# Optimization experiments

Hardware: AMD Instinct MI355X
Metric: run time of the kernel (lower is better)

## Reference

```python
import jax, jax.numpy as jnp
import numpy as np

D, H, WIN, TEMP = 512, 8, 2, 1.0
DH = D // H
SCALE = DH ** -0.5
SHIFT = WIN // 2


def _ln(x, g, b):
    m = jnp.mean(x, -1, keepdims=True)
    v = jnp.mean(jnp.square(x - m), -1, keepdims=True)
    return (x - m) * jax.lax.rsqrt(v + 1e-5) * g + b


def _win_attn(q, k, v):
    a = jax.nn.softmax(jnp.einsum('nhqd,nhkd->nhqk', q * SCALE, k) / TEMP, axis=-1)
    return jnp.einsum('nhqk,nhkd->nhqd', a, v)


def _self_block(x, p):
    qkv_w, qkv_b, proj_w, proj_b, n1g, n1b, n2g, n2b = p
    b, t, d = x.shape
    sc = x
    xw = _ln(x, n1g, n1b).reshape(b * t // WIN, WIN, d)  # window partition
    qkv = (xw @ qkv_w + qkv_b).reshape(-1, WIN, 3, H, DH).transpose(2, 0, 3, 1, 4)
    o = _win_attn(qkv[0], qkv[1], qkv[2])
    o = o.transpose(0, 2, 1, 3).reshape(-1, WIN, d) @ proj_w + proj_b
    return _ln(o.reshape(b, t, d) + sc, n2g, n2b)  # window reverse + residual


def _self_tf(x, p):
    x = _self_block(x, p)
    x = jnp.roll(x, -SHIFT, axis=1)   # sequence_shift
    x = _self_block(x, p)
    return jnp.roll(x, SHIFT, axis=1)  # sequence_inverse_shift


def _cross_block(x, y, p):
    q_w, q_b, kv_w, kv_b, proj_w, proj_b, n1g, n1b, n2g, n2b = p
    b, t, d = x.shape
    sc = x
    xw = _ln(x, n1g, n1b).reshape(-1, WIN, d)
    yw = _ln(y, n1g, n1b).reshape(-1, WIN, d)  # shared pre_norm, as in source
    q = (xw @ q_w + q_b).reshape(-1, WIN, H, DH).transpose(0, 2, 1, 3)
    kv = (yw @ kv_w + kv_b).reshape(-1, WIN, 2, H, DH).transpose(2, 0, 3, 1, 4)
    o = _win_attn(q, kv[0], kv[1])
    o = o.transpose(0, 2, 1, 3).reshape(-1, WIN, d) @ proj_w + proj_b
    return _ln(o.reshape(b, t, d) + sc, n2g, n2b)


def _cross_tf(x, y, p):
    x = _cross_block(x, y, p)
    x = jnp.roll(x, -SHIFT, axis=1)
    x = _cross_block(x, jnp.roll(y, -SHIFT, axis=1), p)
    return jnp.roll(x, SHIFT, axis=1)


def setup_inputs() -> dict:
    key = jax.random.key(0)
    ks = iter(jax.random.split(key, 40))
    B, T = 16, 4096
    d = {
        'x': jax.random.normal(next(ks), (B, T, D), jnp.float32),
        'y': jax.random.normal(next(ks), (B, T, D), jnp.float32),
    }

    def w(shape):
        return jax.random.normal(next(ks), shape, jnp.float32) * 0.02

    for m in ('wa', 'wv'):  # within-modal audio / video
        d[m + '_qkv_w'] = w((D, 3 * D)); d[m + '_qkv_b'] = jnp.zeros((3 * D,), jnp.float32)
        d[m + '_proj_w'] = w((D, D));    d[m + '_proj_b'] = jnp.zeros((D,), jnp.float32)
        d[m + '_n1_g'] = jnp.ones((D,), jnp.float32); d[m + '_n1_b'] = jnp.zeros((D,), jnp.float32)
        d[m + '_n2_g'] = jnp.ones((D,), jnp.float32); d[m + '_n2_b'] = jnp.zeros((D,), jnp.float32)
    # shared cross-modal transformer
    d['cm_q_w'] = w((D, D));      d['cm_q_b'] = jnp.zeros((D,), jnp.float32)
    d['cm_kv_w'] = w((D, 2 * D)); d['cm_kv_b'] = jnp.zeros((2 * D,), jnp.float32)
    d['cm_proj_w'] = w((D, D));   d['cm_proj_b'] = jnp.zeros((D,), jnp.float32)
    d['cm_n1_g'] = jnp.ones((D,), jnp.float32); d['cm_n1_b'] = jnp.zeros((D,), jnp.float32)
    d['cm_n2_g'] = jnp.ones((D,), jnp.float32); d['cm_n2_b'] = jnp.zeros((D,), jnp.float32)
    return d


def reference(x, y,
              wa_qkv_w, wa_qkv_b, wa_proj_w, wa_proj_b, wa_n1_g, wa_n1_b, wa_n2_g, wa_n2_b,
              wv_qkv_w, wv_qkv_b, wv_proj_w, wv_proj_b, wv_n1_g, wv_n1_b, wv_n2_g, wv_n2_b,
              cm_q_w, cm_q_b, cm_kv_w, cm_kv_b, cm_proj_w, cm_proj_b, cm_n1_g, cm_n1_b, cm_n2_g, cm_n2_b):
    pa = (wa_qkv_w, wa_qkv_b, wa_proj_w, wa_proj_b, wa_n1_g, wa_n1_b, wa_n2_g, wa_n2_b)
    pv = (wv_qkv_w, wv_qkv_b, wv_proj_w, wv_proj_b, wv_n1_g, wv_n1_b, wv_n2_g, wv_n2_b)
    pc = (cm_q_w, cm_q_b, cm_kv_w, cm_kv_b, cm_proj_w, cm_proj_b, cm_n1_g, cm_n1_b, cm_n2_g, cm_n2_b)
    # args.s1_attn == 'all' path
    x = _self_tf(x, pa)
    y = _self_tf(y, pv)
    xc = _cross_tf(x, y, pc)
    yc = _cross_tf(y, x, pc)
    return jnp.stack([x + xc, y + yc])  # (2, B, T, D)
```

## Files before the change

kernel.cpp:

```cpp
#include <hip/hip_runtime.h>

typedef unsigned short u16;
typedef unsigned int u32;
typedef __attribute__((ext_vector_type(8))) short short8;
typedef __attribute__((ext_vector_type(4))) short short4v;
typedef __attribute__((ext_vector_type(4))) float f32x4;

#define D_MODEL 512
#define NH 8
#define TSEQ 4096
#define NB 16
#define NROWS (NB*TSEQ)
#define QK_SCALE 0.125f
#define KDIM 512
#define NKI (KDIM/32)

__device__ __forceinline__ float b2f(u16 u){
    union { float f; unsigned int i; } v; v.i = ((unsigned int)u) << 16; return v.f;
}
__device__ __forceinline__ u16 f2b(float f){
    union { float f; unsigned int i; } v; v.f = f;
    unsigned int r = v.i + 0x7FFFu + ((v.i >> 16) & 1u);
    return (u16)(r >> 16);
}

__device__ __forceinline__ void async_copy16(u16* lds, const u16* g){
    __builtin_amdgcn_global_load_lds(
        (const __attribute__((address_space(1))) u32*)g,
        (__attribute__((address_space(3))) u32*)lds, 16, 0, 0);
}

__global__ void wconv_kernel(const float* __restrict__ W, u16* __restrict__ Wt, int K, int N){
    int idx = blockIdx.x * 256 + threadIdx.x;
    if (idx >= K * N) return;
    int n = idx / K;
    int k = idx - n * K;
    Wt[idx] = f2b(W[(size_t)k * N + n]);
}

__global__ __launch_bounds__(256) void ln_kernel(
    const float* __restrict__ X, const float* __restrict__ g,
    const float* __restrict__ b, u16* __restrict__ out)
{
    int row  = blockIdx.x * 4 + (threadIdx.x >> 6);
    int lane = threadIdx.x & 63;
    size_t base = (size_t)row * D_MODEL + lane * 8;
    float4 x0 = *(const float4*)(X + base);
    float4 x1 = *(const float4*)(X + base + 4);
    float t[8] = {x0.x,x0.y,x0.z,x0.w,x1.x,x1.y,x1.z,x1.w};
    float s = 0.f, ss = 0.f;
    #pragma unroll
    for (int j = 0; j < 8; j++){ s += t[j]; ss += t[j]*t[j]; }
    #pragma unroll
    for (int m = 1; m < 64; m <<= 1){ s += __shfl_xor(s, m); ss += __shfl_xor(ss, m); }
    float mean = s * (1.f/D_MODEL);
    float var  = ss * (1.f/D_MODEL) - mean*mean;
    float rst  = rsqrtf(var + 1e-5f);
    float4 g0 = *(const float4*)(g + lane*8);
    float4 g1 = *(const float4*)(g + lane*8 + 4);
    float4 c0 = *(const float4*)(b + lane*8);
    float4 c1 = *(const float4*)(b + lane*8 + 4);
    float gv[8] = {g0.x,g0.y,g0.z,g0.w,g1.x,g1.y,g1.z,g1.w};
    float bv[8] = {c0.x,c0.y,c0.z,c0.w,c1.x,c1.y,c1.z,c1.w};
    short8 o;
    #pragma unroll
    for (int j = 0; j < 8; j++) o[j] = (short)f2b((t[j]-mean)*rst*gv[j] + bv[j]);
    *(short8*)(out + base) = o;
}

__global__ __launch_bounds__(256) void resln_kernel(
    const u16* __restrict__ P, const float* __restrict__ Xin,
    const float* __restrict__ Add,
    const float* __restrict__ g, const float* __restrict__ b,
    float* __restrict__ out,
    u16* __restrict__ lnout, const float* __restrict__ g2, const float* __restrict__ b2)
{
    int row  = blockIdx.x * 4 + (threadIdx.x >> 6);
    int lane = threadIdx.x & 63;
    size_t base = (size_t)row * D_MODEL + lane * 8;
    short8 pv = *(const short8*)(P + base);
    float4 x0 = *(const float4*)(Xin + base);
    float4 x1 = *(const float4*)(Xin + base + 4);
    float xr[8] = {x0.x,x0.y,x0.z,x0.w,x1.x,x1.y,x1.z,x1.w};
    float t[8];
    #pragma unroll
    for (int j = 0; j < 8; j++) t[j] = b2f((u16)pv[j]) + xr[j];
    float s = 0.f, ss = 0.f;
    #pragma unroll
    for (int j = 0; j < 8; j++){ s += t[j]; ss += t[j]*t[j]; }
    #pragma unroll
    for (int m = 1; m < 64; m <<= 1){ s += __shfl_xor(s, m); ss += __shfl_xor(ss, m); }
    float mean = s * (1.f/D_MODEL);
    float var  = ss * (1.f/D_MODEL) - mean*mean;
    float rst  = rsqrtf(var + 1e-5f);
    float4 g0 = *(const float4*)(g + lane*8);
    float4 g1 = *(const float4*)(g + lane*8 + 4);
    float4 c0 = *(const float4*)(b + lane*8);
    float4 c1 = *(const float4*)(b + lane*8 + 4);
    float gv[8] = {g0.x,g0.y,g0.z,g0.w,g1.x,g1.y,g1.z,g1.w};
    float bv[8] = {c0.x,c0.y,c0.z,c0.w,c1.x,c1.y,c1.z,c1.w};
    float lnb[8], o[8];
    #pragma unroll
    for (int j = 0; j < 8; j++){ lnb[j] = (t[j]-mean)*rst; o[j] = lnb[j]*gv[j] + bv[j]; }

    if (lnout){
        float s2 = 0.f, ss2 = 0.f;
        #pragma unroll
        for (int j = 0; j < 8; j++){ s2 += o[j]; ss2 += o[j]*o[j]; }
        #pragma unroll
        for (int m = 1; m < 64; m <<= 1){ s2 += __shfl_xor(s2, m); ss2 += __shfl_xor(ss2, m); }
        float mean2 = s2 * (1.f/D_MODEL);
        float var2  = ss2 * (1.f/D_MODEL) - mean2*mean2;
        float rst2  = rsqrtf(var2 + 1e-5f);
        float4 g20 = *(const float4*)(g2 + lane*8);
        float4 g21 = *(const float4*)(g2 + lane*8 + 4);
        float4 b20 = *(const float4*)(b2 + lane*8);
        float4 b21 = *(const float4*)(b2 + lane*8 + 4);
        float g2v[8] = {g20.x,g20.y,g20.z,g20.w,g21.x,g21.y,g21.z,g21.w};
        float b2v[8] = {b20.x,b20.y,b20.z,b20.w,b21.x,b21.y,b21.z,b21.w};
        short8 lo;
        #pragma unroll
        for (int j = 0; j < 8; j++) lo[j] = (short)f2b((o[j]-mean2)*rst2*g2v[j] + b2v[j]);
        *(short8*)(lnout + base) = lo;
    }
    if (Add){
        float4 a0 = *(const float4*)(Add + base);
        float4 a1 = *(const float4*)(Add + base + 4);
        float av[8] = {a0.x,a0.y,a0.z,a0.w,a1.x,a1.y,a1.z,a1.w};
        #pragma unroll
        for (int j = 0; j < 8; j++) o[j] += av[j];
    }
    float4 r0 = {o[0],o[1],o[2],o[3]};
    float4 r1 = {o[4],o[5],o[6],o[7]};
    *(float4*)(out + base)     = r0;
    *(float4*)(out + base + 4) = r1;
}

__global__ __launch_bounds__(256) void qkvattn_kernel(
    const u16* __restrict__ A, const u16* __restrict__ Wt,
    const float* __restrict__ bias, u16* __restrict__ O, int shift)
{
    __shared__ __align__(16) u16 lds[2][20*512];
    int tid  = threadIdx.x;
    int lane = tid & 63;
    int wid  = tid >> 6;

    int bid  = blockIdx.x;
    int swz  = (bid & 7) * 512 + (bid >> 3);
    int head = swz >> 9;
    int rt   = swz & 511;
    int bt   = rt >> 5;
    int tb   = (rt & 31) * 128;

    f32x4 acc[2][12];
    f32x4 zero = {0.f,0.f,0.f,0.f};
    #pragma unroll
    for (int m = 0; m < 2; m++)
        #pragma unroll
        for (int n = 0; n < 12; n++) acc[m][n] = zero;

    int rr = lane >> 2, kc = (lane & 3) * 8;
    const u16* p[5];
    int cidb = wid * 5;
    #pragma unroll
    for (int q = 0; q < 5; q++){
        int cid = cidb + q;
        if (cid < 8){
            int i   = cid*16 + rr;
            int tok = (tb + shift + i) & (TSEQ-1);
            p[q] = A + ((size_t)bt * TSEQ + tok) * KDIM + kc;
        } else {
            int cb   = cid - 8;
            int wrow = (cb >> 2) * 512 + head*64 + (cb & 3)*16 + rr;
            p[q] = Wt + (size_t)wrow * KDIM + kc;
        }
    }

    int lrow = lane & 15;
    int lk   = (lane >> 4) * 8;
    int aoff = (wid*32 + lrow) * 32 + lk;
    int boff = 8*512 + lrow*32 + lk;

    #pragma unroll
    for (int q = 0; q < 5; q++){ async_copy16(&lds[0][(cidb+q)*512], p[q]); p[q] += 32; }
    asm volatile("s_waitcnt vmcnt(0)" ::: "memory");
    __syncthreads();

    #pragma unroll
    for (int t = 0; t < NKI; t++){
        const u16* cbuf = lds[t & 1];
        u16* nbuf = (u16*)lds[(t & 1) ^ 1];
        if (t < NKI-1){
            #pragma unroll
            for (int q = 0; q < 5; q++){ async_copy16(&nbuf[(cidb+q)*512], p[q]); p[q] += 32; }
        }
        short8 af[2], bf[12];
        #pragma unroll
        for (int m = 0; m < 2; m++) af[m] = *(const short8*)(cbuf + aoff + m*512);
        #pragma unroll
        for (int n = 0; n < 12; n++) bf[n] = *(const short8*)(cbuf + boff + n*512);
        #pragma unroll
        for (int m = 0; m < 2; m++)
            #pragma unroll
            for (int n = 0; n < 12; n++)
                acc[m][n] = __builtin_amdgcn_mfma_f32_16x16x32_bf16(af[m], bf[n], acc[m][n], 0, 0, 0);
        if (t < NKI-1){
            asm volatile("s_waitcnt vmcnt(0)" ::: "memory");
            __syncthreads();
        }
    }

    int g_ = lane >> 4, lc = lane & 15;
    float bq[4], bk[4], bv[4];
    #pragma unroll
    for (int n = 0; n < 4; n++){
        int d = head*64 + n*16 + lc;
        bq[n] = bias[d]; bk[n] = bias[512 + d]; bv[n] = bias[1024 + d];
    }
    #pragma unroll
    for (int m = 0; m < 2; m++){
        #pragma unroll
        for (int wnd = 0; wnd < 2; wnd++){
            int ja = 2*wnd, jb = ja + 1;
            float s00=0.f, s01=0.f, s10=0.f, s11=0.f;
            #pragma unroll
            for (int n = 0; n < 4; n++){
                float qa = acc[m][n][ja] + bq[n],  qb = acc[m][n][jb] + bq[n];
                float ka = acc[m][4+n][ja] + bk[n], kb = acc[m][4+n][jb] + bk[n];
                s00 += qa*ka; s01 += qa*kb; s10 += qb*ka; s11 += qb*kb;
            }
            #pragma unroll
            for (int msk = 1; msk < 16; msk <<= 1){
                s00 += __shfl_xor(s00, msk); s01 += __shfl_xor(s01, msk);
                s10 += __shfl_xor(s10, msk); s11 += __shfl_xor(s11, msk);
            }
            s00 *= QK_SCALE; s01 *= QK_SCALE; s10 *= QK_SCALE; s11 *= QK_SCALE;
            float m0 = fmaxf(s00, s01), m1 = fmaxf(s10, s11);
            float e00 = expf(s00-m0), e01 = expf(s01-m0);
            float e10 = expf(s10-m1), e11 = expf(s11-m1);
            float ia = 1.f/(e00+e01), ib = 1.f/(e10+e11);
            float a00 = e00*ia, a01 = e01*ia, a10 = e10*ib, a11 = e11*ib;
            int ra = wid*32 + m*16 + 4*g_ + ja;
            int ta = (tb + shift + ra) & (TSEQ-1);
            size_t growa = (size_t)bt * TSEQ + ta;
            size_t growb = (size_t)bt * TSEQ + ((ta + 1) & (TSEQ-1));
            #pragma unroll
            for (int n = 0; n < 4; n++){
                float va = acc[m][8+n][ja] + bv[n], vb = acc[m][8+n][jb] + bv[n];
                int col = head*64 + n*16 + lc;
                O[growa * D_MODEL + col] = f2b(a00*va + a01*vb);
                O[growb * D_MODEL + col] = f2b(a10*va + a11*vb);
            }
        }
    }
}

#define BM 128
#define BN 128

__global__ __launch_bounds__(256) void gemm_kernel(
    const u16* __restrict__ A, const u16* __restrict__ Wt,
    const float* __restrict__ bias, u16* __restrict__ C,
    int N, int nN)
{
    __shared__ __align__(16) u16 lds[2][16*512];
    int tid  = threadIdx.x;
    int lane = tid & 63;
    int wid  = tid >> 6;
    int wm = wid >> 1, wn = wid & 1;

    int cpx = (int)gridDim.x >> 3;
    int swz = ((int)blockIdx.x & 7) * cpx + ((int)blockIdx.x >> 3);
    int row0 = (swz / nN) * BM;
    int col0 = (swz % nN) * BN;

    f32x4 acc[4][4];
    f32x4 zero = {0.f,0.f,0.f,0.f};
    #pragma unroll
    for (int i = 0; i < 4; i++)
        #pragma unroll
        for (int j = 0; j < 4; j++) acc[i][j] = zero;

    int rr = lane >> 2, kc = (lane & 3) * 8;
    const u16* p[4];
    int cidb = wid * 4;
    #pragma unroll
    for (int q = 0; q < 4; q++){
        int cid = cidb + q;
        if (cid < 8) p[q] = A  + (size_t)(row0 + cid*16 + rr) * KDIM + kc;
        else         p[q] = Wt + (size_t)(col0 + (cid-8)*16 + rr) * KDIM + kc;
    }

    int lrow = lane & 15;
    int lk   = (lane >> 4) * 8;
    int aoff = (wm*64 + lrow) * 32 + lk;
    int boff = 8*512 + (wn*64 + lrow) * 32 + lk;

    #pragma unroll
    for (int q = 0; q < 4; q++){ async_copy16(&lds[0][(cidb+q)*512], p[q]); p[q] += 32; }
    asm volatile("s_waitcnt vmcnt(0)" ::: "memory");
    __syncthreads();

    #pragma unroll
    for (int t = 0; t < NKI; t++){
        const u16* cbuf = lds[t & 1];
        u16* nbuf = (u16*)lds[(t & 1) ^ 1];
        if (t < NKI-1){
            #pragma unroll
            for (int q = 0; q < 4; q++){ async_copy16(&nbuf[(cidb+q)*512], p[q]); p[q] += 32; }
        }
        short8 af[4], bf[4];
        #pragma unroll
        for (int m = 0; m < 4; m++) af[m] = *(const short8*)(cbuf + aoff + m*512);
        #pragma unroll
        for (int n = 0; n < 4; n++) bf[n] = *(const short8*)(cbuf + boff + n*512);
        #pragma unroll
        for (int m = 0; m < 4; m++)
            #pragma unroll
            for (int n = 0; n < 4; n++)
                acc[m][n] = __builtin_amdgcn_mfma_f32_16x16x32_bf16(af[m], bf[n], acc[m][n], 0, 0, 0);
        if (t < NKI-1){
            asm volatile("s_waitcnt vmcnt(0)" ::: "memory");
            __syncthreads();
        }
    }

    int lr4 = (lane >> 4) * 4;
    int lc  = lane & 15;
    #pragma unroll
    for (int n = 0; n < 4; n++) {
        int c = col0 + wn*64 + n*16 + lc;
        float bvv = bias[c];
        #pragma unroll
        for (int m = 0; m < 4; m++) {
            int r = row0 + wm*64 + m*16 + lr4;
            f32x4 v = acc[m][n];
            C[(size_t)(r+0) * N + c] = f2b(v[0] + bvv);
            C[(size_t)(r+1) * N + c] = f2b(v[1] + bvv);
            C[(size_t)(r+2) * N + c] = f2b(v[2] + bvv);
            C[(size_t)(r+3) * N + c] = f2b(v[3] + bvv);
        }
    }
}

__global__ __launch_bounds__(256) void attn_cross_kernel(
    const u16* __restrict__ Q, const u16* __restrict__ KV,
    u16* __restrict__ O, int shift)
{
    int tsk  = blockIdx.x * 4 + (threadIdx.x >> 6);
    int lane = threadIdx.x & 63;
    int w  = tsk >> 1;
    int hb = tsk & 1;
    int bt = w >> 11;
    int wt = w & 2047;
    int t0 = (2*wt + shift) & (TSEQ - 1);
    int t1 = (t0 + 1) & (TSEQ - 1);
    size_t g0 = (size_t)bt * TSEQ + t0;
    size_t g1 = (size_t)bt * TSEQ + t1;
    int col = hb*256 + lane*4;
    short4v q0 = *(const short4v*)(Q  + g0*512  + col);
    short4v q1 = *(const short4v*)(Q  + g1*512  + col);
    short4v k0 = *(const short4v*)(KV + g0*1024 + col);
    short4v k1 = *(const short4v*)(KV + g1*1024 + col);
    short4v v0 = *(const short4v*)(KV + g0*1024 + 512 + col);
    short4v v1 = *(const short4v*)(KV + g1*1024 + 512 + col);
    float s00=0.f, s01=0.f, s10=0.f, s11=0.f;
    float v0f[4], v1f[4];
    #pragma unroll
    for (int j = 0; j < 4; j++){
        float qa = b2f((u16)q0[j]), qb = b2f((u16)q1[j]);
        float ka = b2f((u16)k0[j]), kb = b2f((u16)k1[j]);
        v0f[j] = b2f((u16)v0[j]); v1f[j] = b2f((u16)v1[j]);
        s00 += qa*ka; s01 += qa*kb; s10 += qb*ka; s11 += qb*kb;
    }
    #pragma unroll
    for (int m = 1; m < 16; m <<= 1){
        s00 += __shfl_xor(s00, m); s01 += __shfl_xor(s01, m);
        s10 += __shfl_xor(s10, m); s11 += __shfl_xor(s11, m);
    }
    s00 *= QK_SCALE; s01 *= QK_SCALE; s10 *= QK_SCALE; s11 *= QK_SCALE;
    float m0 = fmaxf(s00, s01), m1 = fmaxf(s10, s11);
    float e00 = expf(s00 - m0), e01 = expf(s01 - m0);
    float e10 = expf(s10 - m1), e11 = expf(s11 - m1);
    float ia = 1.f/(e00 + e01), ib = 1.f/(e10 + e11);
    float a00 = e00*ia, a01 = e01*ia, a10 = e10*ib, a11 = e11*ib;
    short4v o0, o1;
    #pragma unroll
    for (int j = 0; j < 4; j++){
        o0[j] = (short)f2b(a00*v0f[j] + a01*v1f[j]);
        o1[j] = (short)f2b(a10*v0f[j] + a11*v1f[j]);
    }
    *(short4v*)(O + g0*512 + col) = o0;
    *(short4v*)(O + g1*512 + col) = o1;
}

extern "C" void kernel_launch(void* const* d_in, const int* in_sizes, int n_in,
                              void* d_out, int out_size, void* d_ws, size_t ws_size,
                              hipStream_t stream)
{
    const float* x = (const float*)d_in[0];
    const float* y = (const float*)d_in[1];
    const float* wa_qkv_w = (const float*)d_in[2];  const float* wa_qkv_b = (const float*)d_in[3];
    const float* wa_proj_w= (const float*)d_in[4];  const float* wa_proj_b= (const float*)d_in[5];
    const float* wa_n1g   = (const float*)d_in[6];  const float* wa_n1b   = (const float*)d_in[7];
    const float* wa_n2g   = (const float*)d_in[8];  const float* wa_n2b   = (const float*)d_in[9];
    const float* wv_qkv_w = (const float*)d_in[10]; const float* wv_qkv_b = (const float*)d_in[11];
    const float* wv_proj_w= (const float*)d_in[12]; const float* wv_proj_b= (const float*)d_in[13];
    const float* wv_n1g   = (const float*)d_in[14]; const float* wv_n1b   = (const float*)d_in[15];
    const float* wv_n2g   = (const float*)d_in[16]; const float* wv_n2b   = (const float*)d_in[17];
    const float* cm_q_w   = (const float*)d_in[18]; const float* cm_q_b   = (const float*)d_in[19];
    const float* cm_kv_w  = (const float*)d_in[20]; const float* cm_kv_b  = (const float*)d_in[21];
    const float* cm_proj_w= (const float*)d_in[22]; const float* cm_proj_b= (const float*)d_in[23];
    const float* cm_n1g   = (const float*)d_in[24]; const float* cm_n1b   = (const float*)d_in[25];
    const float* cm_n2g   = (const float*)d_in[26]; const float* cm_n2b   = (const float*)d_in[27];

    char* ws = (char*)d_ws;
    const size_t SZ_F32 = (size_t)NROWS * D_MODEL * 4;
    const size_t SZ_B16 = (size_t)NROWS * D_MODEL * 2;
    float* F1  = (float*)(ws);
    float* XF  = (float*)(ws + SZ_F32);
    float* YF  = (float*)(ws + 2*SZ_F32);
    u16*   XN  = (u16*)  (ws + 3*SZ_F32);
    u16*   CN  = (u16*)  (ws + 3*SZ_F32 + SZ_B16);
    u16*   XLN = (u16*)  (ws + 3*SZ_F32 + 2*SZ_B16);
    u16*   YLN = (u16*)  (ws + 3*SZ_F32 + 3*SZ_B16);
    u16*   O   = (u16*)  (ws + 3*SZ_F32 + 4*SZ_B16);
    u16*   KVb = (u16*)  (ws + 3*SZ_F32 + 5*SZ_B16);
    u16*   WB  = (u16*)  (ws + 3*SZ_F32 + 8*SZ_B16);

    u16* PB = KVb;

    u16* wa_qkv_t  = WB;
    u16* wa_proj_t = wa_qkv_t  + 1536*512;
    u16* wv_qkv_t  = wa_proj_t + 512*512;
    u16* wv_proj_t = wv_qkv_t  + 1536*512;
    u16* cm_q_t    = wv_proj_t + 512*512;
    u16* cm_kv_t   = cm_q_t    + 512*512;
    u16* cm_proj_t = cm_kv_t   + 1024*512;

    auto conv = [&](const float* W, u16* Wt, int K, int N){
        int total = K * N;
        wconv_kernel<<<(total + 255) / 256, 256, 0, stream>>>(W, Wt, K, N);
    };
    conv(wa_qkv_w,  wa_qkv_t,  512, 1536);
    conv(wa_proj_w, wa_proj_t, 512, 512);
    conv(wv_qkv_w,  wv_qkv_t,  512, 1536);
    conv(wv_proj_w, wv_proj_t, 512, 512);
    conv(cm_q_w,    cm_q_t,    512, 512);
    conv(cm_kv_w,   cm_kv_t,   512, 1024);
    conv(cm_proj_w, cm_proj_t, 512, 512);

    const int lnGrid   = NROWS / 4;
    const int attnGrid = NROWS / 2 * 2 / 4;
    const int qaGrid   = (NROWS / 128) * NH;

    auto gemm = [&](const u16* Ain, const u16* Wt, const float* bias, u16* Cout, int N){
        int nN = N / BN;
        gemm_kernel<<<(NROWS/BM) * nN, 256, 0, stream>>>(Ain, Wt, bias, Cout, N, nN);
    };

    auto self_chain = [&](const float* in, float* outF, u16* outLN,
                          const u16* qkvT, const float* qkv_b,
                          const u16* projT, const float* proj_b,
                          const float* n1g, const float* n1b,
                          const float* n2g, const float* n2b){
        ln_kernel<<<lnGrid, 256, 0, stream>>>(in, n1g, n1b, XN);
        qkvattn_kernel<<<qaGrid, 256, 0, stream>>>(XN, qkvT, qkv_b, O, 0);
        gemm(O, projT, proj_b, PB, 512);
        resln_kernel<<<lnGrid, 256, 0, stream>>>(PB, in, nullptr, n2g, n2b, F1, XN, n1g, n1b);
        qkvattn_kernel<<<qaGrid, 256, 0, stream>>>(XN, qkvT, qkv_b, O, 1);
        gemm(O, projT, proj_b, PB, 512);
        resln_kernel<<<lnGrid, 256, 0, stream>>>(PB, F1, nullptr, n2g, n2b, outF, outLN, cm_n1g, cm_n1b);
    };

    self_chain(x, XF, XLN, wa_qkv_t, wa_qkv_b, wa_proj_t, wa_proj_b, wa_n1g, wa_n1b, wa_n2g, wa_n2b);
    self_chain(y, YF, YLN, wv_qkv_t, wv_qkv_b, wv_proj_t, wv_proj_b, wv_n1g, wv_n1b, wv_n2g, wv_n2b);

    float* out0 = (float*)d_out;
    float* out1 = out0 + (size_t)NROWS * D_MODEL;

    auto cross_chain = [&](const u16* qLN, const u16* kvLN, const float* resF, float* outF){
        gemm(kvLN, cm_kv_t, cm_kv_b, KVb, 1024);
        gemm(qLN,  cm_q_t,  cm_q_b,  XN,  512);
        attn_cross_kernel<<<attnGrid, 256, 0, stream>>>(XN, KVb, O, 0);
        gemm(O, cm_proj_t, cm_proj_b, XN, 512);
        resln_kernel<<<lnGrid, 256, 0, stream>>>(XN, resF, nullptr, cm_n2g, cm_n2b, F1, CN, cm_n1g, cm_n1b);
        gemm(CN, cm_q_t, cm_q_b, XN, 512);
        attn_cross_kernel<<<attnGrid, 256, 0, stream>>>(XN, KVb, O, 1);
        gemm(O, cm_proj_t, cm_proj_b, XN, 512);
        resln_kernel<<<lnGrid, 256, 0, stream>>>(XN, F1, resF, cm_n2g, cm_n2b, outF, nullptr, nullptr, nullptr);
    };

    cross_chain(XLN, YLN, XF, out0);
    cross_chain(YLN, XLN, YF, out1);
}
```

Measured before the change: 2.372 ms.

## Replace 128x128 GEMM with 256x256 tiled, swizzled-LDS, 512-thread kernel

Replaces the projection GEMM with a kernel that computes 256x256 output tiles using 8 waves. Each wave holds an 8x4 grid of MFMA accumulators, and each pipeline stage loads K=64. LDS rows are XOR-swizzled to reduce bank conflicts, loads use a partial vmcnt wait, and MFMA issue is raised with setprio. The goal is more data reuse per loaded byte and fewer sync points per K step. In exchange it uses 128KB of LDS and more registers, which lowers occupancy, and it launches fewer blocks.

After: 2.495 ms. +5.2%, slower.

```diff
diff --git a/kernel.cpp b/kernel.cpp
--- a/kernel.cpp
+++ b/kernel.cpp
@@ -99,9 +99,9 @@
     float4 c1 = *(const float4*)(b + lane*8 + 4);
     float gv[8] = {g0.x,g0.y,g0.z,g0.w,g1.x,g1.y,g1.z,g1.w};
     float bv[8] = {c0.x,c0.y,c0.z,c0.w,c1.x,c1.y,c1.z,c1.w};
-    float lnb[8], o[8];
-    #pragma unroll
-    for (int j = 0; j < 8; j++){ lnb[j] = (t[j]-mean)*rst; o[j] = lnb[j]*gv[j] + bv[j]; }
+    float o[8];
+    #pragma unroll
+    for (int j = 0; j < 8; j++) o[j] = (t[j]-mean)*rst*gv[j] + bv[j];
 
     if (lnout){
         float s2 = 0.f, ss2 = 0.f;
@@ -255,85 +255,101 @@
     }
 }
 
-#define BM 128
-#define BN 128
-
-__global__ __launch_bounds__(256) void gemm_kernel(
+__global__ __launch_bounds__(512) void gemm256_kernel(
     const u16* __restrict__ A, const u16* __restrict__ Wt,
-    const float* __restrict__ bias, u16* __restrict__ C,
-    int N, int nN)
+    const float* __restrict__ bias, u16* __restrict__ C, int N, int nN)
 {
-    __shared__ __align__(16) u16 lds[2][16*512];
+    __shared__ __align__(16) u16 sh[65536];
     int tid  = threadIdx.x;
     int lane = tid & 63;
     int wid  = tid >> 6;
-    int wm = wid >> 1, wn = wid & 1;
+    int wm   = wid >> 2, wn = wid & 3;
 
     int cpx = (int)gridDim.x >> 3;
     int swz = ((int)blockIdx.x & 7) * cpx + ((int)blockIdx.x >> 3);
-    int row0 = (swz / nN) * BM;
-    int col0 = (swz % nN) * BN;
-
-    f32x4 acc[4][4];
+    int row0 = (swz / nN) * 256;
+    int col0 = (swz % nN) * 256;
+
+    f32x4 acc[8][4];
     f32x4 zero = {0.f,0.f,0.f,0.f};
     #pragma unroll
-    for (int i = 0; i < 4; i++)
-        #pragma unroll
-        for (int j = 0; j < 4; j++) acc[i][j] = zero;
-
-    int rr = lane >> 2, kc = (lane & 3) * 8;
-    const u16* p[4];
-    int cidb = wid * 4;
-    #pragma unroll
-    for (int q = 0; q < 4; q++){
-        int cid = cidb + q;
-        if (cid < 8) p[q] = A  + (size_t)(row0 + cid*16 + rr) * KDIM + kc;
-        else         p[q] = Wt + (size_t)(col0 + (cid-8)*16 + rr) * KDIM + kc;
-    }
-
-    int lrow = lane & 15;
-    int lk   = (lane >> 4) * 8;
-    int aoff = (wm*64 + lrow) * 32 + lk;
-    int boff = 8*512 + (wn*64 + lrow) * 32 + lk;
-
-    #pragma unroll
-    for (int q = 0; q < 4; q++){ async_copy16(&lds[0][(cidb+q)*512], p[q]); p[q] += 32; }
-    asm volatile("s_waitcnt vmcnt(0)" ::: "memory");
-    __syncthreads();
-
-    #pragma unroll
-    for (int t = 0; t < NKI; t++){
-        const u16* cbuf = lds[t & 1];
-        u16* nbuf = (u16*)lds[(t & 1) ^ 1];
-        if (t < NKI-1){
-            #pragma unroll
-            for (int q = 0; q < 4; q++){ async_copy16(&nbuf[(cidb+q)*512], p[q]); p[q] += 32; }
+    for (int m = 0; m < 8; m++)
+        #pragma unroll
+        for (int n = 0; n < 4; n++) acc[m][n] = zero;
+
+    int lrow = lane & 15, khi = lane >> 4;
+    int addrA[8], addrB[4];
+    #pragma unroll
+    for (int m = 0; m < 8; m++){
+        int r = wm*128 + m*16 + lrow;
+        addrA[m] = r*32 + ((khi ^ ((r>>1)&3)) << 3);
+    }
+    #pragma unroll
+    for (int n = 0; n < 4; n++){
+        int r = wn*64 + n*16 + lrow;
+        addrB[n] = r*32 + ((khi ^ ((r>>1)&3)) << 3);
+    }
+
+    const u16* Ab = A  + (size_t)row0 * KDIM;
+    const u16* Bb = Wt + (size_t)col0 * KDIM;
+    int sr0 = (wid << 4) + (lane >> 2);
+    int ss  = lane & 3;
+    int sx  = (ss ^ ((sr0 >> 1) & 3)) << 3;
+
+    #define STAGE_A(buf, t, kh) { \
+        u16* d_ = &sh[(buf)*16384 + (kh)*8192 + wid*512]; \
+        const u16* s_ = Ab + (size_t)sr0*KDIM + (t)*64 + (kh)*32 + sx; \
+        async_copy16(d_, s_); \
+        async_copy16(d_ + 4096, s_ + (size_t)128*KDIM); }
+    #define STAGE_B(buf, t, kh) { \
+        u16* d_ = &sh[32768 + (buf)*16384 + (kh)*8192 + wid*512]; \
+        const u16* s_ = Bb + (size_t)sr0*KDIM + (t)*64 + (kh)*32 + sx; \
+        async_copy16(d_, s_); \
+        async_copy16(d_ + 4096, s_ + (size_t)128*KDIM); }
+
+    #define COMPUTE(buf, kh) { \
+        const u16* ca_ = &sh[(buf)*16384 + (kh)*8192]; \
+        const u16* cb_ = ca_ + 32768; \
+        short8 af[8], bf[4]; \
+        _Pragma("unroll") \
+        for (int m = 0; m < 8; m++) af[m] = *(const short8*)(ca_ + addrA[m]); \
+        _Pragma("unroll") \
+        for (int n = 0; n < 4; n++) bf[n] = *(const short8*)(cb_ + addrB[n]); \
+        __builtin_amdgcn_s_setprio(1); \
+        _Pragma("unroll") \
+        for (int m = 0; m < 8; m++) \
+            _Pragma("unroll") \
+            for (int n = 0; n < 4; n++) \
+                acc[m][n] = __builtin_amdgcn_mfma_f32_16x16x32_bf16(af[m], bf[n], acc[m][n], 0, 0, 0); \
+        __builtin_amdgcn_s_setprio(0); }
+
+    STAGE_A(0, 0, 0); STAGE_B(0, 0, 0);
+    STAGE_A(0, 0, 1); STAGE_B(0, 0, 1);
+
+    #pragma unroll
+    for (int t = 0; t < 8; t++){
+        int buf = t & 1;
+        if (t < 7){
+            STAGE_A(buf^1, t+1, 0); STAGE_B(buf^1, t+1, 0);
+            STAGE_A(buf^1, t+1, 1); STAGE_B(buf^1, t+1, 1);
+            asm volatile("s_waitcnt vmcnt(8)" ::: "memory");
+        } else {
+            asm volatile("s_waitcnt vmcnt(0)" ::: "memory");
         }
-        short8 af[4], bf[4];
-        #pragma unroll
-        for (int m = 0; m < 4; m++) af[m] = *(const short8*)(cbuf + aoff + m*512);
-        #pragma unroll
-        for (int n = 0; n < 4; n++) bf[n] = *(const short8*)(cbuf + boff + n*512);
-        #pragma unroll
-        for (int m = 0; m < 4; m++)
-            #pragma unroll
-            for (int n = 0; n < 4; n++)
-                acc[m][n] = __builtin_amdgcn_mfma_f32_16x16x32_bf16(af[m], bf[n], acc[m][n], 0, 0, 0);
-        if (t < NKI-1){
-            asm volatile("s_waitcnt vmcnt(0)" ::: "memory");
-            __syncthreads();
-        }
-    }
-
-    int lr4 = (lane >> 4) * 4;
-    int lc  = lane & 15;
-    #pragma unroll
-    for (int n = 0; n < 4; n++) {
+        __builtin_amdgcn_s_barrier();
+        COMPUTE(buf, 0);
+        COMPUTE(buf, 1);
+        __builtin_amdgcn_s_barrier();
+    }
+
+    int g_ = lane >> 4, lc = lane & 15;
+    #pragma unroll
+    for (int n = 0; n < 4; n++){
         int c = col0 + wn*64 + n*16 + lc;
         float bvv = bias[c];
         #pragma unroll
-        for (int m = 0; m < 4; m++) {
-            int r = row0 + wm*64 + m*16 + lr4;
+        for (int m = 0; m < 8; m++){
+            int r = row0 + wm*128 + m*16 + 4*g_;
             f32x4 v = acc[m][n];
             C[(size_t)(r+0) * N + c] = f2b(v[0] + bvv);
             C[(size_t)(r+1) * N + c] = f2b(v[1] + bvv);
@@ -341,6 +357,9 @@
             C[(size_t)(r+3) * N + c] = f2b(v[3] + bvv);
         }
     }
+    #undef STAGE_A
+    #undef STAGE_B
+    #undef COMPUTE
 }
 
 __global__ __launch_bounds__(256) void attn_cross_kernel(
@@ -455,8 +474,8 @@
     const int qaGrid   = (NROWS / 128) * NH;
 
     auto gemm = [&](const u16* Ain, const u16* Wt, const float* bias, u16* Cout, int N){
-        int nN = N / BN;
-        gemm_kernel<<<(NROWS/BM) * nN, 256, 0, stream>>>(Ain, Wt, bias, Cout, N, nN);
+        int nN = N / 256;
+        gemm256_kernel<<<(NROWS/256) * nN, 512, 0, stream>>>(Ain, Wt, bias, Cout, N, nN);
     };
 
     auto self_chain = [&](const float* in, float* outF, u16* outLN,
```
